# Kernel optimization log

Measured on AMD Instinct MI355X. Metric: run time of the kernel, lower is better.

Reference implementation:

```python
import jax, jax.numpy as jnp
import numpy as np

SIGMA = 0.1
H = 32
M_, L_, N_, D_ = 4, 6, 320, 2


def setup_inputs() -> dict:
    key = jax.random.key(0)
    ks = jax.random.split(key, 10)
    data = jax.random.normal(ks[0], (M_, L_, N_, D_), dtype=jnp.float32)
    t_snapshots = jnp.arange(L_, dtype=jnp.float32)
    s = 0.5  # mild scale so tanh MLPs stay in their smooth regime
    return {
        'data': data,
        't_snapshots': t_snapshots,
        'V_w1': jax.random.normal(ks[1], (D_, H), dtype=jnp.float32) * s,
        'V_b1': jax.random.normal(ks[2], (H,), dtype=jnp.float32) * s,
        'V_w2': jax.random.normal(ks[3], (H, 1), dtype=jnp.float32) * s,
        'V_b2': jax.random.normal(ks[4], (1,), dtype=jnp.float32) * s,
        'Phi_w1': jax.random.normal(ks[5], (H,), dtype=jnp.float32) * s,
        'Phi_b1': jax.random.normal(ks[6], (H,), dtype=jnp.float32) * s,
        'Phi_w2': jax.random.normal(ks[7], (H,), dtype=jnp.float32) * s,
        'Phi_b2': jax.random.normal(ks[8], (1,), dtype=jnp.float32) * s,
    }


def _forward(data, t_snapshots, V_w1, V_b1, V_w2, V_b2, Phi_w1, Phi_b1, Phi_w2, Phi_b2):
    sigma_sq = SIGMA ** 2
    M, L, N, d = data.shape
    B = M * (L - 1)
    dt = t_snapshots[1:] - t_snapshots[:-1]                     # (L-1,)
    X_curr = data[:, :-1].reshape(B, N, d)
    X_next = data[:, 1:].reshape(B, N, d)
    dt_exp = jnp.broadcast_to(dt[None, :], (M, L - 1)).reshape(B)

    def v_scalar(x):  # (d,) -> scalar potential V
        return jnp.dot(jnp.tanh(x @ V_w1 + V_b1), V_w2[:, 0]) + V_b2[0]

    def phi_scalar(r):  # scalar -> scalar interaction Phi
        return jnp.dot(jnp.tanh(r * Phi_w1 + Phi_b1), Phi_w2) + Phi_b2[0]

    eye = jnp.eye(N, dtype=bool)
    off = (~eye).astype(data.dtype)  # zero-out self-pairs (diagonal mask)

    def pairwise(X):
        diff = X[:, :, None, :] - X[:, None, :, :]              # (B,N,N,d)
        sq = jnp.sum(diff * diff, axis=-1)                       # (B,N,N)
        dist = jnp.sqrt(jnp.where(sq > 0, sq, 1.0))              # grad-safe sqrt
        dist = jnp.where(sq > 0, dist, 0.0)
        return diff, dist

    # --- one-body terms: grad V and Laplacian V ---
    X_flat = X_curr.reshape(B * N, d)
    grad_V = jax.vmap(jax.grad(v_scalar))(X_flat).reshape(B, N, d)
    lap_V = jax.vmap(lambda x: jnp.trace(jax.hessian(v_scalar)(x)))(X_flat).reshape(B, N)

    # --- pairwise terms: Phi', Phi'' on all distances ---
    diff, dist = pairwise(X_curr)
    dist_safe = jnp.maximum(dist, 1e-10)
    rf = dist.reshape(-1)
    dPhi = jax.vmap(jax.grad(phi_scalar))(rf).reshape(B, N, N)
    d2Phi = jax.vmap(jax.grad(jax.grad(phi_scalar)))(rf).reshape(B, N, N)

    unit_diff = diff / dist_safe[..., None]
    grad_Phi_pairs = dPhi[..., None] * unit_diff * off[None, :, :, None]
    drift = -grad_V - grad_Phi_pairs.sum(axis=2) / N            # (B,N,d)

    if d == 1:
        lap_Phi = d2Phi
    else:
        lap_Phi = d2Phi + (d - 1) / dist_safe * dPhi
    lap_Phi = lap_Phi * off[None]
    lap_sum = lap_V + lap_Phi.sum(axis=2) / N                   # (B,N)

    # --- energy E(X) = mean V + mean_offdiag Phi ---
    def energy(X):
        Xf = X.reshape(-1, d)
        V_vals = (jnp.tanh(Xf @ V_w1 + V_b1) @ V_w2)[:, 0] + V_b2[0]
        V_mean = V_vals.reshape(X.shape[0], N).mean(axis=1)
        _, dd = pairwise(X)
        Phi_vals = jnp.tanh(dd[..., None] * Phi_w1 + Phi_b1) @ Phi_w2 + Phi_b2[0]
        Phi_vals = Phi_vals * off[None]
        return V_mean + Phi_vals.sum(axis=(1, 2)) / (N * N)

    E_curr = energy(X_curr)
    E_next = energy(X_next)

    J_diss = (drift ** 2).sum(axis=(1, 2)) / N * dt_exp
    J_diff = sigma_sq * lap_sum.mean(axis=1) * dt_exp
    J_energy = E_next - E_curr
    n_pairs = B
    residual = J_diss.sum() / n_pairs + J_diff.sum() / n_pairs - 2.0 * J_energy.sum() / n_pairs
    return residual ** 2


def reference(data, t_snapshots, V_w1, V_b1, V_w2, V_b2, Phi_w1, Phi_b1, Phi_w2, Phi_b2):
    return _forward(data, t_snapshots, V_w1, V_b1, V_w2, V_b2, Phi_w1, Phi_b1, Phi_w2, Phi_b2)
```

## Files before the change

### kernel.cpp

```cpp
#include <hip/hip_runtime.h>

#define NP   320
#define HD   32
#define MT   4
#define LS   6
#define BB   (MT * (LS - 1))
#define NCFG (MT * LS)
#define ROWS (NCFG * NP)
#define SIG2 0.01f
#define L2E2 2.8853900817779268f

#define NCELL 1024
#define RMAX  12.0f
#define TSCALE ((float)NCELL / RMAX)
#define CWID   (RMAX / (float)NCELL)

#define OFF_T12 0
#define OFF_T3  2056
#define OFF_S0  4096
#define OFF_S1  (4096 + ROWS)

__device__ __forceinline__ float fexp2(float x){ return __builtin_amdgcn_exp2f(x); }
__device__ __forceinline__ float frcp(float x){ return __builtin_amdgcn_rcpf(x); }
__device__ __forceinline__ float frsq(float x){ return __builtin_amdgcn_rsqf(x); }

__global__ __launch_bounds__(1024) void build_table_kernel(
    const float* __restrict__ Phi_w1, const float* __restrict__ Phi_b1,
    const float* __restrict__ Phi_w2, float* __restrict__ ws)
{
    float2* t12 = (float2*)(ws + OFF_T12);
    float*  t3  = ws + OFF_T3;
    for (int c = threadIdx.x; c < NCELL + 1; c += 1024) {
        float rr = (float)c * CWID;
        float f1 = 0.0f, f2 = 0.0f, f3 = 0.0f;
        #pragma unroll
        for (int h = 0; h < HD; ++h) {
            float w  = Phi_w1[h];
            float bb = Phi_b1[h];
            float w2 = Phi_w2[h];
            float e  = fexp2(fmaf(rr, w, bb) * L2E2);
            float rc = frcp(e + 1.0f);
            float u  = fmaf(-rc, rc, rc);
            float t  = fmaf(-2.0f, rc, 1.0f);
            f1 = fmaf(u,     4.0f * w * w2,        f1);
            f2 = fmaf(u * t, -8.0f * w * w * w2,   f2);
            f3 = fmaf(t, w2, f3);
        }
        t12[c] = make_float2(f1, f2);
        t3[c]  = f3;
    }
}

__global__ __launch_bounds__(256) void main_kernel(
    const float* __restrict__ data,
    const float* __restrict__ t_snap,
    const float* __restrict__ V_w1,
    const float* __restrict__ V_b1,
    const float* __restrict__ V_w2,
    const float* __restrict__ V_b2,
    const float* __restrict__ Phi_b2,
    float* __restrict__ ws)
{
    __shared__ float2 sT12[NCELL + 1];
    __shared__ float  sT3[NCELL + 1];
    __shared__ float2 sX[NP];

    const int tid  = threadIdx.x;
    const int lane = tid & 63;
    const int wid  = tid >> 6;
    const int row0 = blockIdx.x * 4;
    const int cfg  = row0 / NP;
    const int l    = cfg % LS;

    {
        const float2* gT12 = (const float2*)(ws + OFF_T12);
        const float*  gT3  = ws + OFF_T3;
        const float2* Xg   = (const float2*)(data + (size_t)cfg * NP * 2);
        for (int c = tid; c < NCELL + 1; c += 256) {
            sT12[c] = gT12[c];
            sT3[c]  = gT3[c];
        }
        for (int c = tid; c < NP; c += 256) sX[c] = Xg[c];
    }
    __syncthreads();

    const int i = row0 + wid - cfg * NP;
    const float2 xi = sX[i];

    float gx = 0.0f, gy = 0.0f, lp = 0.0f, ph = 0.0f;
    #pragma unroll
    for (int k = 0; k < NP / 64; ++k) {
        const int j = lane + 64 * k;
        const float2 xj = sX[j];
        const float d0 = xi.x - xj.x;
        const float d1 = xi.y - xj.y;
        const float sq = fmaf(d1, d1, d0 * d0);
        const float inv = frsq(sq);
        const float r   = sq * inv;
        float x = fminf(r * TSCALE, (float)NCELL - 0.001f);
        const int   i0 = (int)x;
        const float fr = x - (float)i0;
        const float2 a = sT12[i0];
        const float2 b = sT12[i0 + 1];
        const float f1 = fmaf(b.x - a.x, fr, a.x);
        const float f2 = fmaf(b.y - a.y, fr, a.y);
        const float f3 = fmaf(sT3[i0 + 1] - sT3[i0], fr, sT3[i0]);
        const float t0 = f1 * inv;
        float cgx = t0 * d0;
        float cgy = t0 * d1;
        float clp = f2 + t0;
        float cph = f3;
        if (j == i) { cgx = 0.0f; cgy = 0.0f; clp = 0.0f; cph = 0.0f; }
        gx += cgx; gy += cgy; lp += clp; ph += cph;
    }
    #pragma unroll
    for (int off = 32; off; off >>= 1) {
        gx += __shfl_down(gx, off, 64);
        gy += __shfl_down(gy, off, 64);
        lp += __shfl_down(lp, off, 64);
        ph += __shfl_down(ph, off, 64);
    }

    float gvx = 0.0f, gvy = 0.0f, lv = 0.0f, vv = 0.0f;
    if (lane < HD) {
        float w0 = V_w1[lane];
        float w1 = V_w1[HD + lane];
        float z  = fmaf(xi.x, w0, fmaf(xi.y, w1, V_b1[lane]));
        float e  = fexp2(z * L2E2);
        float rc = frcp(e + 1.0f);
        float u  = fmaf(-rc, rc, rc);
        float t  = fmaf(-2.0f, rc, 1.0f);
        float v2 = V_w2[lane];
        float cu = 4.0f * u * v2;
        gvx = cu * w0;
        gvy = cu * w1;
        lv  = -8.0f * u * t * v2 * (w0 * w0 + w1 * w1);
        vv  = t * v2;
        #pragma unroll
        for (int off = 16; off; off >>= 1) {
            gvx += __shfl_xor(gvx, off, 64);
            gvy += __shfl_xor(gvy, off, 64);
            lv  += __shfl_xor(lv,  off, 64);
            vv  += __shfl_xor(vv,  off, 64);
        }
    }

    if (lane == 0) {
        const float invN = 1.0f / (float)NP;
        float c0 = 0.0f, c1 = 0.0f;
        if (l < LS - 1) {
            float dx = -gvx - gx * invN;
            float dy = -gvy - gy * invN;
            float lap_sum = lv + lp * invN;
            float dt = t_snap[l + 1] - t_snap[l];
            c0 = dt * (dx * dx + dy * dy) * invN + SIG2 * dt * lap_sum * invN;
        }
        if (l == 0 || l == LS - 1) {
            const float coef = (l == LS - 1) ? 1.0f : -1.0f;
            float v = vv + V_b2[0];
            float P = ph + (float)(NP - 1) * Phi_b2[0];
            c1 = coef * (v * invN + P * invN * invN);
        }
        const int row = row0 + wid;
        ws[OFF_S0 + row] = c0;
        ws[OFF_S1 + row] = c1;
    }
}

__global__ __launch_bounds__(1024) void reduce_kernel(
    const float* __restrict__ ws, float* __restrict__ out)
{
    __shared__ float sR[16][2];
    const int tid = threadIdx.x;
    float a0 = 0.0f, a1 = 0.0f;
    for (int idx = tid; idx < ROWS; idx += 1024) {
        a0 += ws[OFF_S0 + idx];
        a1 += ws[OFF_S1 + idx];
    }
    #pragma unroll
    for (int off = 32; off; off >>= 1) {
        a0 += __shfl_down(a0, off, 64);
        a1 += __shfl_down(a1, off, 64);
    }
    const int lane = tid & 63, wid = tid >> 6;
    if (lane == 0) { sR[wid][0] = a0; sR[wid][1] = a1; }
    __syncthreads();
    if (tid == 0) {
        float S0 = 0.0f, S1 = 0.0f;
        #pragma unroll
        for (int w = 0; w < 16; ++w) { S0 += sR[w][0]; S1 += sR[w][1]; }
        float res = (S0 - 2.0f * S1) / (float)BB;
        out[0] = res * res;
    }
}

extern "C" void kernel_launch(void* const* d_in, const int* in_sizes, int n_in,
                              void* d_out, int out_size, void* d_ws, size_t ws_size,
                              hipStream_t stream) {
    const float* data    = (const float*)d_in[0];
    const float* t_snap  = (const float*)d_in[1];
    const float* V_w1    = (const float*)d_in[2];
    const float* V_b1    = (const float*)d_in[3];
    const float* V_w2    = (const float*)d_in[4];
    const float* V_b2    = (const float*)d_in[5];
    const float* Phi_w1  = (const float*)d_in[6];
    const float* Phi_b1  = (const float*)d_in[7];
    const float* Phi_w2  = (const float*)d_in[8];
    const float* Phi_b2  = (const float*)d_in[9];
    float* ws  = (float*)d_ws;
    float* out = (float*)d_out;

    build_table_kernel<<<1, 1024, 0, stream>>>(Phi_w1, Phi_b1, Phi_w2, ws);

    main_kernel<<<ROWS / 4, 256, 0, stream>>>(
        data, t_snap, V_w1, V_b1, V_w2, V_b2, Phi_b2, ws);

    reduce_kernel<<<1, 1024, 0, stream>>>(ws, out);
}
```

Before: 91.09 us.

## Fuse final reduction into main kernel via slotted atomics and last-block finish

Removes the separate reduce kernel: each block sums its four per-row contributions in shared memory, atomically adds them into one of 32 spread accumulator slots, and the last block (found via an atomic counter) sums the slots and writes the output. The Phi lookup table is halved to 512 cells and packed into one float4 array, so each block loads less shared memory and each interpolation needs fewer LDS reads. The build kernel now zeroes the accumulators and counter. The trade-offs are atomic contention, nondeterministic float summation order, and coarser table interpolation.

```diff
diff --git a/kernel.cpp b/kernel.cpp
--- a/kernel.cpp
+++ b/kernel.cpp
@@ -7,18 +7,19 @@
 #define BB   (MT * (LS - 1))
 #define NCFG (MT * LS)
 #define ROWS (NCFG * NP)
+#define GRID (ROWS / 4)
 #define SIG2 0.01f
 #define L2E2 2.8853900817779268f
 
-#define NCELL 1024
+#define NCELL 512
 #define RMAX  12.0f
 #define TSCALE ((float)NCELL / RMAX)
 #define CWID   (RMAX / (float)NCELL)
 
-#define OFF_T12 0
-#define OFF_T3  2056
-#define OFF_S0  4096
-#define OFF_S1  (4096 + ROWS)
+#define OFF_TAB 0
+#define OFF_ACC 2112
+#define NSLOT   32
+#define OFF_CNT (OFF_ACC + NSLOT * 32)
 
 __device__ __forceinline__ float fexp2(float x){ return __builtin_amdgcn_exp2f(x); }
 __device__ __forceinline__ float frcp(float x){ return __builtin_amdgcn_rcpf(x); }
@@ -28,9 +29,9 @@
     const float* __restrict__ Phi_w1, const float* __restrict__ Phi_b1,
     const float* __restrict__ Phi_w2, float* __restrict__ ws)
 {
-    float2* t12 = (float2*)(ws + OFF_T12);
-    float*  t3  = ws + OFF_T3;
-    for (int c = threadIdx.x; c < NCELL + 1; c += 1024) {
+    float4* tab = (float4*)(ws + OFF_TAB);
+    const int tid = threadIdx.x;
+    for (int c = tid; c < NCELL + 1; c += 1024) {
         float rr = (float)c * CWID;
         float f1 = 0.0f, f2 = 0.0f, f3 = 0.0f;
         #pragma unroll
@@ -42,13 +43,13 @@
             float rc = frcp(e + 1.0f);
             float u  = fmaf(-rc, rc, rc);
             float t  = fmaf(-2.0f, rc, 1.0f);
-            f1 = fmaf(u,     4.0f * w * w2,        f1);
-            f2 = fmaf(u * t, -8.0f * w * w * w2,   f2);
+            f1 = fmaf(u,     4.0f * w * w2,      f1);
+            f2 = fmaf(u * t, -8.0f * w * w * w2, f2);
             f3 = fmaf(t, w2, f3);
         }
-        t12[c] = make_float2(f1, f2);
-        t3[c]  = f3;
-    }
+        tab[c] = make_float4(f1, f2, f3, 0.0f);
+    }
+    for (int c = tid; c < NSLOT * 32 + 1; c += 1024) ws[OFF_ACC + c] = 0.0f;
 }
 
 __global__ __launch_bounds__(256) void main_kernel(
@@ -59,11 +60,13 @@
     const float* __restrict__ V_w2,
     const float* __restrict__ V_b2,
     const float* __restrict__ Phi_b2,
-    float* __restrict__ ws)
+    float* __restrict__ ws,
+    float* __restrict__ out)
 {
-    __shared__ float2 sT12[NCELL + 1];
-    __shared__ float  sT3[NCELL + 1];
+    __shared__ float4 sTab[NCELL + 1];
     __shared__ float2 sX[NP];
+    __shared__ float  sRed[4][2];
+    __shared__ int    sLast;
 
     const int tid  = threadIdx.x;
     const int lane = tid & 63;
@@ -73,18 +76,14 @@
     const int l    = cfg % LS;
 
     {
-        const float2* gT12 = (const float2*)(ws + OFF_T12);
-        const float*  gT3  = ws + OFF_T3;
-        const float2* Xg   = (const float2*)(data + (size_t)cfg * NP * 2);
-        for (int c = tid; c < NCELL + 1; c += 256) {
-            sT12[c] = gT12[c];
-            sT3[c]  = gT3[c];
-        }
+        const float4* gT = (const float4*)(ws + OFF_TAB);
+        const float2* Xg = (const float2*)(data + (size_t)cfg * NP * 2);
+        for (int c = tid; c < NCELL + 1; c += 256) sTab[c] = gT[c];
         for (int c = tid; c < NP; c += 256) sX[c] = Xg[c];
     }
     __syncthreads();
 
-    const int i = row0 + wid - cfg * NP;
+    const int i = row0 - cfg * NP + wid;
     const float2 xi = sX[i];
 
     float gx = 0.0f, gy = 0.0f, lp = 0.0f, ph = 0.0f;
@@ -100,11 +99,11 @@
         float x = fminf(r * TSCALE, (float)NCELL - 0.001f);
         const int   i0 = (int)x;
         const float fr = x - (float)i0;
-        const float2 a = sT12[i0];
-        const float2 b = sT12[i0 + 1];
+        const float4 a = sTab[i0];
+        const float4 b = sTab[i0 + 1];
         const float f1 = fmaf(b.x - a.x, fr, a.x);
         const float f2 = fmaf(b.y - a.y, fr, a.y);
-        const float f3 = fmaf(sT3[i0 + 1] - sT3[i0], fr, sT3[i0]);
+        const float f3 = fmaf(b.z - a.z, fr, a.z);
         const float t0 = f1 * inv;
         float cgx = t0 * d0;
         float cgy = t0 * d1;
@@ -161,36 +160,36 @@
             float P = ph + (float)(NP - 1) * Phi_b2[0];
             c1 = coef * (v * invN + P * invN * invN);
         }
-        const int row = row0 + wid;
-        ws[OFF_S0 + row] = c0;
-        ws[OFF_S1 + row] = c1;
-    }
-}
-
-__global__ __launch_bounds__(1024) void reduce_kernel(
-    const float* __restrict__ ws, float* __restrict__ out)
-{
-    __shared__ float sR[16][2];
-    const int tid = threadIdx.x;
-    float a0 = 0.0f, a1 = 0.0f;
-    for (int idx = tid; idx < ROWS; idx += 1024) {
-        a0 += ws[OFF_S0 + idx];
-        a1 += ws[OFF_S1 + idx];
-    }
-    #pragma unroll
-    for (int off = 32; off; off >>= 1) {
-        a0 += __shfl_down(a0, off, 64);
-        a1 += __shfl_down(a1, off, 64);
-    }
-    const int lane = tid & 63, wid = tid >> 6;
-    if (lane == 0) { sR[wid][0] = a0; sR[wid][1] = a1; }
+        sRed[wid][0] = c0;
+        sRed[wid][1] = c1;
+    }
     __syncthreads();
+
     if (tid == 0) {
-        float S0 = 0.0f, S1 = 0.0f;
+        float S0 = sRed[0][0] + sRed[1][0] + sRed[2][0] + sRed[3][0];
+        float S1 = sRed[0][1] + sRed[1][1] + sRed[2][1] + sRed[3][1];
+        float* slot = ws + OFF_ACC + (blockIdx.x & (NSLOT - 1)) * 32;
+        atomicAdd(slot + 0, S0);
+        atomicAdd(slot + 1, S1);
+        __threadfence();
+        unsigned old = atomicAdd((unsigned*)(ws + OFF_CNT), 1u);
+        sLast = (old == (unsigned)(GRID - 1)) ? 1 : 0;
+    }
+    __syncthreads();
+
+    if (sLast && tid < NSLOT) {
+        __threadfence();
+        float a0 = atomicAdd(ws + OFF_ACC + tid * 32 + 0, 0.0f);
+        float a1 = atomicAdd(ws + OFF_ACC + tid * 32 + 1, 0.0f);
         #pragma unroll
-        for (int w = 0; w < 16; ++w) { S0 += sR[w][0]; S1 += sR[w][1]; }
-        float res = (S0 - 2.0f * S1) / (float)BB;
-        out[0] = res * res;
+        for (int off = 16; off; off >>= 1) {
+            a0 += __shfl_down(a0, off, 64);
+            a1 += __shfl_down(a1, off, 64);
+        }
+        if (tid == 0) {
+            float res = (a0 - 2.0f * a1) / (float)BB;
+            out[0] = res * res;
+        }
     }
 }
 
@@ -212,8 +211,6 @@
 
     build_table_kernel<<<1, 1024, 0, stream>>>(Phi_w1, Phi_b1, Phi_w2, ws);
 
-    main_kernel<<<ROWS / 4, 256, 0, stream>>>(
-        data, t_snap, V_w1, V_b1, V_w2, V_b2, Phi_b2, ws);
-
-    reduce_kernel<<<1, 1024, 0, stream>>>(ws, out);
+    main_kernel<<<GRID, 256, 0, stream>>>(
+        data, t_snap, V_w1, V_b1, V_w2, V_b2, Phi_b2, ws, out);
 }
```

New measurement: 111.4 us. 22.3% more time.
